# Kernel optimization log

Hardware: AMD Instinct MI355X
Metric: run time of the kernel (lower is better)

## Reference

```python
import jax, jax.numpy as jnp
import numpy as np

B, S, D, H = 8, 1024, 1024, 16
DK = D // H


def setup_inputs() -> dict:
    key = jax.random.key(0)
    ks = jax.random.split(key, 10)
    scale = 1.0 / np.sqrt(D)
    return {
        "x": jax.random.normal(ks[0], (B, S, D), dtype=jnp.float32),
        "prefix": jax.random.randint(ks[1], (B,), 0, S, dtype=jnp.int32),
        "Wq": jax.random.normal(ks[2], (D, D), dtype=jnp.float32) * scale,
        "bq": jnp.zeros((D,), dtype=jnp.float32),
        "Wk": jax.random.normal(ks[3], (D, D), dtype=jnp.float32) * scale,
        "bk": jnp.zeros((D,), dtype=jnp.float32),
        "Wv": jax.random.normal(ks[4], (D, D), dtype=jnp.float32) * scale,
        "bv": jnp.zeros((D,), dtype=jnp.float32),
        "Wo": jax.random.normal(ks[5], (D, D), dtype=jnp.float32) * scale,
        "bo": jnp.zeros((D,), dtype=jnp.float32),
    }


def reference(x, prefix, Wq, bq, Wk, bk, Wv, bv, Wo, bo):
    b, s, d = x.shape
    h, dk = H, DK
    # projections -> [b, h, s, dk]
    def split_heads(t):
        return t.reshape(b, s, h, dk).transpose(0, 2, 1, 3)
    q = split_heads(x @ Wq + bq)
    k = split_heads(x @ Wk + bk)
    v = split_heads(x @ Wv + bv)
    # raw scores (no 1/sqrt(dk) scaling in the original)
    scores = jnp.einsum('bhqd,bhkd->bhqk', q, k)
    # mask construction (faithful to original, incl. final permute/transpose):
    # allowed[b, q, k] = (q < prefix[b]) or (k >= q)
    q_idx = jnp.arange(s)[:, None]   # [s, 1]
    k_idx = jnp.arange(s)[None, :]   # [1, s]
    allowed = (q_idx[None, :, :] < prefix[:, None, None]) | (k_idx >= q_idx)  # [b, s, s]
    scores = jnp.where(allowed[:, None, :, :], scores, -jnp.inf)
    probs = jax.nn.softmax(scores, axis=-1)
    # einsum -> bqhd, then transpose(1,2) -> bhqd, then view(b, s, d) (faithful
    # to the original's head-interleaving reshape)
    out = jnp.einsum('bhql,bhld->bqhd', probs, v)
    out = out.transpose(0, 2, 1, 3).reshape(b, s, d)
    return out @ Wo + bo
```

## Files before the change

kernel.cpp:

```cpp
#include <hip/hip_runtime.h>
#include <stdint.h>

typedef __attribute__((ext_vector_type(8)))  short          short8;
typedef __attribute__((ext_vector_type(8)))  unsigned short u16x8;
typedef __attribute__((ext_vector_type(4)))  unsigned short u16x4;
typedef __attribute__((ext_vector_type(4)))  float          f32x4;
typedef __attribute__((ext_vector_type(16))) float          f32x16;

__device__ __forceinline__ unsigned short f2bf(float x) {
  unsigned int u = __float_as_uint(x);
  u += 0x7fffu + ((u >> 16) & 1u);
  return (unsigned short)(u >> 16);
}
__device__ __forceinline__ float bf2f(unsigned short b) {
  return __uint_as_float(((unsigned int)b) << 16);
}

__device__ __forceinline__ void mfma16(f32x4& c, short8 a, short8 b) {
  asm volatile("v_mfma_f32_16x16x32_bf16 %0, %1, %2, %0" : "+v"(c) : "v"(a), "v"(b));
}
__device__ __forceinline__ void mfma32(f32x16& c, short8 a, short8 b) {
  asm volatile("v_mfma_f32_32x32x16_bf16 %0, %1, %2, %0" : "+v"(c) : "v"(a), "v"(b));
}
__device__ __forceinline__ float hw_exp2(float x) {
  float r;
  asm("v_exp_f32 %0, %1" : "=v"(r) : "v"(x));
  return r;
}

#define GLDS(gsrc, ldst)                                                    \
  __builtin_amdgcn_global_load_lds(                                         \
      (const __attribute__((address_space(1))) void*)(gsrc),                \
      (__attribute__((address_space(3))) void*)(ldst), 16, 0, 0)

__global__ void split_x_kernel(const float4* __restrict__ x,
                               ushort4* __restrict__ xh, int n4) {
  int stride = gridDim.x * blockDim.x;
  for (int i = blockIdx.x * blockDim.x + threadIdx.x; i < n4; i += stride) {
    float4 v = x[i];
    ushort4 h;
    h.x = f2bf(v.x);
    h.y = f2bf(v.y);
    h.z = f2bf(v.z);
    h.w = f2bf(v.w);
    xh[i] = h;
  }
}

__global__ void wsplit_kernel(const float* __restrict__ Wq, const float* __restrict__ Wk,
                              const float* __restrict__ Wv, const float* __restrict__ Wo,
                              unsigned short* qk, unsigned short* vh, unsigned short* oh) {
  __shared__ float tile[32][33];
  int z = blockIdx.z;
  const float* W = (z == 0) ? Wq : (z == 1) ? Wk : (z == 2) ? Wv : Wo;
  unsigned short* Oh = (z == 0) ? qk : (z == 1) ? qk + (size_t)1024 * 1024
                      : (z == 2) ? vh : oh;
  int k0 = blockIdx.y * 32, n0 = blockIdx.x * 32;
  int tx = threadIdx.x & 31, ty = threadIdx.x >> 5;
#pragma unroll
  for (int j = 0; j < 4; ++j)
    tile[ty + 8 * j][tx] = W[(size_t)(k0 + ty + 8 * j) * 1024 + n0 + tx];
  __syncthreads();
#pragma unroll
  for (int j = 0; j < 4; ++j) {
    float v = tile[tx][ty + 8 * j];
    size_t idx = (size_t)(n0 + ty + 8 * j) * 1024 + k0 + tx;
    Oh[idx] = f2bf(v);
  }
}

template <int OUTMODE>
__global__ __launch_bounds__(256)
void gemm_kernel(const unsigned short* __restrict__ Ah,
                 const unsigned short* __restrict__ Bh,
                 const float* __restrict__ bias, const float* __restrict__ bias2,
                 unsigned short* __restrict__ Ch,
                 float* __restrict__ Cf, int M, int N, int K) {
  constexpr int SMEM = (OUTMODE == 3) ? (128 * 136) : (2 * 8192);
  __shared__ unsigned short smem[SMEM];
  unsigned short* sAh = smem;
  unsigned short* sBh = smem + 8192;

  int t = threadIdx.x;
  int wid = t >> 6, l = t & 63;
  int wm = wid >> 1, wn = wid & 1;
  int bm = blockIdx.y * 128, bn = blockIdx.x * 128;

  f32x4 acc[4][4] = {};

  for (int k0 = 0; k0 < K; k0 += 64) {
#pragma unroll
    for (int r = 0; r < 4; ++r) {
      int o = (r * 256 + t) << 4;
      int row = o >> 7;
      int gce = ((o & 127) ^ ((row & 7) << 4)) >> 1;
      int wb  = (o & ~1023) >> 1;
      size_t gA = (size_t)(bm + row) * K + k0 + gce;
      size_t gB = (size_t)(bn + row) * K + k0 + gce;
      GLDS(Ah + gA, sAh + wb);
      GLDS(Bh + gB, sBh + wb);
    }
    __syncthreads();
#pragma unroll
    for (int kh = 0; kh < 2; ++kh) {
      short8 afh[4], bfh[4];
#pragma unroll
      for (int m = 0; m < 4; ++m) {
        int row = wm * 64 + m * 16 + (l & 15);
        int cb = (((l >> 4) * 16 + kh * 64) ^ ((row & 7) << 4)) >> 1;
        afh[m] = *(const short8*)(sAh + row * 64 + cb);
      }
#pragma unroll
      for (int n = 0; n < 4; ++n) {
        int row = wn * 64 + n * 16 + (l & 15);
        int cb = (((l >> 4) * 16 + kh * 64) ^ ((row & 7) << 4)) >> 1;
        bfh[n] = *(const short8*)(sBh + row * 64 + cb);
      }
#pragma unroll
      for (int m = 0; m < 4; ++m)
#pragma unroll
        for (int n = 0; n < 4; ++n)
          mfma16(acc[m][n], afh[m], bfh[n]);
    }
    __syncthreads();
  }

  if (OUTMODE == 3) {
    unsigned short* sT = smem;
#pragma unroll
    for (int m = 0; m < 4; ++m) {
      int lrow0 = wm * 64 + m * 16 + (l >> 4) * 4;
#pragma unroll
      for (int n = 0; n < 4; ++n) {
        int lcol = wn * 64 + n * 16 + (l & 15);
        float bs = bias[bn + lcol];
        u16x4 w;
#pragma unroll
        for (int r = 0; r < 4; ++r) w[r] = f2bf(acc[m][n][r] + bs);
        *(u16x4*)&sT[lcol * 136 + lrow0] = w;
      }
    }
    __syncthreads();
#pragma unroll
    for (int j = 0; j < 8; ++j) {
      int c = (t >> 4) + 16 * j;
      int r = (t & 15) * 8;
      *(u16x8*)(Ch + (size_t)(bn + c) * M + bm + r) = *(const u16x8*)&sT[c * 136 + r];
    }
    return;
  }

#pragma unroll
  for (int m = 0; m < 4; ++m) {
    int grow0 = bm + wm * 64 + m * 16 + (l >> 4) * 4;
#pragma unroll
    for (int n = 0; n < 4; ++n) {
      int gcol = bn + wn * 64 + n * 16 + (l & 15);
      float bs = (bias2 && gcol >= 1024) ? bias2[gcol - 1024] : bias[gcol];
#pragma unroll
      for (int r = 0; r < 4; ++r) {
        float v = acc[m][n][r] + bs;
        size_t idx = (size_t)(grow0 + r) * N + gcol;
        if (OUTMODE == 2) Cf[idx] = v;
        else              Ch[idx] = f2bf(v);
      }
    }
  }
}

__global__ __launch_bounds__(128)
void attn_kernel(const unsigned short* __restrict__ QK,
                 const unsigned short* __restrict__ VT, const int* __restrict__ prefix,
                 unsigned short* __restrict__ AOh) {
  const float NEG = -3.0e38f;
  const float L2E = 1.4426950408889634f;
  const float MC  = 46.16624410f;
  __shared__ unsigned short sKh[2][32][66];
  __shared__ unsigned short sV [2][64][34];

  int bh = blockIdx.x;
  int b = bh >> 4, h = bh & 15;
  int t = threadIdx.x, wid = t >> 6, l = t & 63;
  int qb0 = blockIdx.y * 64;
  int qb = qb0 + wid * 32;
  int P = prefix[b];
  int lq = l & 31, g = l >> 5;
  int q = qb + lq;
  bool qfull = (q < P);
  bool allfull = (P >= qb + 32);

  short8 bqh[4];
  {
    size_t base = (size_t)(b * 1024 + q) * 2048 + h * 64 + g * 8;
#pragma unroll
    for (int c = 0; c < 4; ++c)
      bqh[c] = *(const short8*)(QK + base + c * 16);
  }

  const unsigned short* KhB = QK + (size_t)b * 1024 * 2048 + 1024 + h * 64;
  const unsigned short* VTB = VT + (size_t)(h * 64) * 8192 + b * 1024;

  int srow = t >> 3, scol = (t & 7) * 8;
  int vrow = t >> 2, vcol = (t & 3) * 8;

  int kt0 = (qb0 >= P) ? qb0 : 0;
  int ntiles = (1024 - kt0) >> 5;

  f32x16 o0 = {}, o1 = {};
  float lrun = 0.f;

  u16x8 rkh0, rkh1, rv0, rv1;
  rkh0 = *(const u16x8*)(KhB + (size_t)(kt0 + srow) * 2048 + scol);
  rkh1 = *(const u16x8*)(KhB + (size_t)(kt0 + srow + 16) * 2048 + scol);
  rv0  = *(const u16x8*)(VTB + (size_t)vrow * 8192 + kt0 + vcol);
  rv1  = *(const u16x8*)(VTB + (size_t)(vrow + 32) * 8192 + kt0 + vcol);
  *(u16x8*)&sKh[0][srow][scol]      = rkh0;
  *(u16x8*)&sKh[0][srow + 16][scol] = rkh1;
  *(u16x8*)&sV [0][vrow][vcol]      = rv0;
  *(u16x8*)&sV [0][vrow + 32][vcol] = rv1;
  __syncthreads();

  int cur = 0;
  for (int i = 0; i < ntiles; ++i) {
    int kt = kt0 + i * 32;
    bool more = (i + 1 < ntiles);
    if (more) {
      int ktn = kt + 32;
      rkh0 = *(const u16x8*)(KhB + (size_t)(ktn + srow) * 2048 + scol);
      rkh1 = *(const u16x8*)(KhB + (size_t)(ktn + srow + 16) * 2048 + scol);
      rv0  = *(const u16x8*)(VTB + (size_t)vrow * 8192 + ktn + vcol);
      rv1  = *(const u16x8*)(VTB + (size_t)(vrow + 32) * 8192 + ktn + vcol);
    }

    bool wave_dead = (qb >= P) && (kt + 31 < qb);
    if (!wave_dead) {
      f32x16 s = {};
      __builtin_amdgcn_s_setprio(1);
#pragma unroll
      for (int c = 0; c < 4; ++c) {
        short8 ah = *(const short8*)&sKh[cur][lq][g * 8 + c * 16];
        mfma32(s, ah, bqh[c]);
      }
      __builtin_amdgcn_s_setprio(0);

      float p[16];
      if (allfull || kt > qb) {
#pragma unroll
        for (int r = 0; r < 16; ++r)
          p[r] = hw_exp2(__builtin_fmaf(s[r], L2E, -MC));
      } else {
#pragma unroll
        for (int r = 0; r < 16; ++r) {
          int k = kt + (r & 3) + 8 * (r >> 2) + 4 * g;
          float sv = (qfull || k >= q) ? s[r] : NEG;
          p[r] = hw_exp2(__builtin_fmaf(sv, L2E, -MC));
        }
      }
      float s01 = p[0] + p[1],  s23 = p[2] + p[3],  s45 = p[4] + p[5],  s67 = p[6] + p[7];
      float s89 = p[8] + p[9],  sab = p[10] + p[11], scd = p[12] + p[13], sef = p[14] + p[15];
      lrun += ((s01 + s23) + (s45 + s67)) + ((s89 + sab) + (scd + sef));

      unsigned int w0, w1, w2, w3, w4, w5, w6, w7;
      asm("v_cvt_pk_bf16_f32 %0, %1, %2" : "=v"(w0) : "v"(p[0]),  "v"(p[1]));
      asm("v_cvt_pk_bf16_f32 %0, %1, %2" : "=v"(w1) : "v"(p[2]),  "v"(p[3]));
      asm("v_cvt_pk_bf16_f32 %0, %1, %2" : "=v"(w2) : "v"(p[4]),  "v"(p[5]));
      asm("v_cvt_pk_bf16_f32 %0, %1, %2" : "=v"(w3) : "v"(p[6]),  "v"(p[7]));
      asm("v_cvt_pk_bf16_f32 %0, %1, %2" : "=v"(w4) : "v"(p[8]),  "v"(p[9]));
      asm("v_cvt_pk_bf16_f32 %0, %1, %2" : "=v"(w5) : "v"(p[10]), "v"(p[11]));
      asm("v_cvt_pk_bf16_f32 %0, %1, %2" : "=v"(w6) : "v"(p[12]), "v"(p[13]));
      asm("v_cvt_pk_bf16_f32 %0, %1, %2" : "=v"(w7) : "v"(p[14]), "v"(p[15]));
      {
        unsigned int v0 = g ? w0 : w2, r0 = __shfl_xor(v0, 32);
        unsigned int v1 = g ? w1 : w3, r1 = __shfl_xor(v1, 32);
        unsigned int v4 = g ? w4 : w6, r4 = __shfl_xor(v4, 32);
        unsigned int v5 = g ? w5 : w7, r5 = __shfl_xor(v5, 32);
        unsigned int n0 = g ? r0 : w0, n2 = g ? w2 : r0;
        unsigned int n1 = g ? r1 : w1, n3 = g ? w3 : r1;
        unsigned int n4 = g ? r4 : w4, n6 = g ? w6 : r4;
        unsigned int n5 = g ? r5 : w5, n7 = g ? w7 : r5;
        w0 = n0; w1 = n1; w2 = n2; w3 = n3; w4 = n4; w5 = n5; w6 = n6; w7 = n7;
      }
      union { unsigned int u[4]; short8 v; } B0, B1;
      B0.u[0] = w0; B0.u[1] = w1; B0.u[2] = w2; B0.u[3] = w3;
      B1.u[0] = w4; B1.u[1] = w5; B1.u[2] = w6; B1.u[3] = w7;

      short8 va00 = *(const short8*)&sV[cur][lq][g * 8];
      short8 va01 = *(const short8*)&sV[cur][lq][16 + g * 8];
      short8 va10 = *(const short8*)&sV[cur][32 + lq][g * 8];
      short8 va11 = *(const short8*)&sV[cur][32 + lq][16 + g * 8];
      __builtin_amdgcn_s_setprio(1);
      mfma32(o0, va00, B0.v);
      mfma32(o0, va01, B1.v);
      mfma32(o1, va10, B0.v);
      mfma32(o1, va11, B1.v);
      __builtin_amdgcn_s_setprio(0);
    }

    if (more) {
      *(u16x8*)&sKh[cur ^ 1][srow][scol]      = rkh0;
      *(u16x8*)&sKh[cur ^ 1][srow + 16][scol] = rkh1;
      *(u16x8*)&sV [cur ^ 1][vrow][vcol]      = rv0;
      *(u16x8*)&sV [cur ^ 1][vrow + 32][vcol] = rv1;
    }
    __syncthreads();
    cur ^= 1;
  }

  lrun += __shfl_xor(lrun, 32);

  float inv = 1.0f / lrun;
  size_t obase = (size_t)(b * 1024 + h * 64 + (q >> 4)) * 1024 + (q & 15) * 64;
#pragma unroll
  for (int tt = 0; tt < 4; ++tt) {
    u16x4 w0, w1;
#pragma unroll
    for (int j = 0; j < 4; ++j) {
      w0[j] = f2bf(o0[4 * tt + j] * inv);
      w1[j] = f2bf(o1[4 * tt + j] * inv);
    }
    *(u16x4*)(AOh + obase + 8 * tt + 4 * g)      = w0;
    *(u16x4*)(AOh + obase + 32 + 8 * tt + 4 * g) = w1;
  }
}

extern "C" void kernel_launch(void* const* d_in, const int* in_sizes, int n_in,
                              void* d_out, int out_size, void* d_ws, size_t ws_size,
                              hipStream_t stream) {
  (void)in_sizes; (void)n_in; (void)out_size;
  const float* x      = (const float*)d_in[0];
  const int*   prefix = (const int*)d_in[1];
  const float* Wq = (const float*)d_in[2];
  const float* bq = (const float*)d_in[3];
  const float* Wk = (const float*)d_in[4];
  const float* bk = (const float*)d_in[5];
  const float* Wv = (const float*)d_in[6];
  const float* bv = (const float*)d_in[7];
  const float* Wo = (const float*)d_in[8];
  const float* bo = (const float*)d_in[9];
  float* out = (float*)d_out;

  const size_t MBY = 1ull << 20;
  if (ws_size < 144 * MBY) return;
  char* ws = (char*)d_ws;
  unsigned short* xh   = (unsigned short*)(ws + 0 * MBY);
  unsigned short* wqk  = (unsigned short*)(ws + 32 * MBY);
  unsigned short* wvh  = (unsigned short*)(ws + 40 * MBY);
  unsigned short* woh  = (unsigned short*)(ws + 44 * MBY);
  unsigned short* QK   = (unsigned short*)(ws + 48 * MBY);
  unsigned short* AOh  = (unsigned short*)(ws + 112 * MBY);
  unsigned short* VT   = (unsigned short*)(ws + 128 * MBY);

  split_x_kernel<<<1024, 256, 0, stream>>>((const float4*)x, (ushort4*)xh, 8192 * 1024 / 4);
  wsplit_kernel<<<dim3(32, 32, 4), 256, 0, stream>>>(Wq, Wk, Wv, Wo, wqk, wvh, woh);
  gemm_kernel<0><<<dim3(16, 64), 256, 0, stream>>>(xh, wqk, bq, bk, QK, nullptr,
                                                   8192, 2048, 1024);
  gemm_kernel<3><<<dim3(8, 64), 256, 0, stream>>>(xh, wvh, bv, nullptr, VT, nullptr,
                                                  8192, 1024, 1024);
  attn_kernel<<<dim3(128, 16), 128, 0, stream>>>(QK, VT, prefix, AOh);
  gemm_kernel<2><<<dim3(8, 64), 256, 0, stream>>>(AOh, woh, bo, nullptr, nullptr, out,
                                                  8192, 1024, 1024);
}
```

Measured before the change: 180.2 us.

## Fuse QKV projection GEMMs into one launch and deepen attention K/V prefetch

Combines the Q/K and V projection GEMMs into a single kernel over a concatenated weight buffer, branching on column block to write either the row-major QK output or the transposed V output. The attention loop now prefetches K/V tiles two iterations ahead using two alternating register sets, to hide global load latency further. This reduces launch count and tail imbalance, at the cost of more registers in attention and larger shared memory in the QK path.

```diff
diff --git a/kernel.cpp b/kernel.cpp
--- a/kernel.cpp
+++ b/kernel.cpp
@@ -49,12 +49,11 @@
 
 __global__ void wsplit_kernel(const float* __restrict__ Wq, const float* __restrict__ Wk,
                               const float* __restrict__ Wv, const float* __restrict__ Wo,
-                              unsigned short* qk, unsigned short* vh, unsigned short* oh) {
+                              unsigned short* qkv, unsigned short* oh) {
   __shared__ float tile[32][33];
   int z = blockIdx.z;
   const float* W = (z == 0) ? Wq : (z == 1) ? Wk : (z == 2) ? Wv : Wo;
-  unsigned short* Oh = (z == 0) ? qk : (z == 1) ? qk + (size_t)1024 * 1024
-                      : (z == 2) ? vh : oh;
+  unsigned short* Oh = (z < 3) ? qkv + (size_t)z * 1024 * 1024 : oh;
   int k0 = blockIdx.y * 32, n0 = blockIdx.x * 32;
   int tx = threadIdx.x & 31, ty = threadIdx.x >> 5;
 #pragma unroll
@@ -69,17 +68,16 @@
   }
 }
 
-template <int OUTMODE>
 __global__ __launch_bounds__(256)
-void gemm_kernel(const unsigned short* __restrict__ Ah,
-                 const unsigned short* __restrict__ Bh,
-                 const float* __restrict__ bias, const float* __restrict__ bias2,
-                 unsigned short* __restrict__ Ch,
-                 float* __restrict__ Cf, int M, int N, int K) {
-  constexpr int SMEM = (OUTMODE == 3) ? (128 * 136) : (2 * 8192);
-  __shared__ unsigned short smem[SMEM];
+void qkv_gemm_kernel(const unsigned short* __restrict__ Ah,
+                     const unsigned short* __restrict__ Bh,
+                     const float* __restrict__ bq, const float* __restrict__ bk,
+                     const float* __restrict__ bv,
+                     unsigned short* __restrict__ QK, unsigned short* __restrict__ VT) {
+  __shared__ unsigned short smem[128 * 136];
   unsigned short* sAh = smem;
   unsigned short* sBh = smem + 8192;
+  const int K = 1024, M = 8192;
 
   int t = threadIdx.x;
   int wid = t >> 6, l = t & 63;
@@ -125,7 +123,8 @@
     __syncthreads();
   }
 
-  if (OUTMODE == 3) {
+  if (bn >= 2048) {
+    int vb = bn - 2048;
     unsigned short* sT = smem;
 #pragma unroll
     for (int m = 0; m < 4; ++m) {
@@ -133,7 +132,7 @@
 #pragma unroll
       for (int n = 0; n < 4; ++n) {
         int lcol = wn * 64 + n * 16 + (l & 15);
-        float bs = bias[bn + lcol];
+        float bs = bv[vb + lcol];
         u16x4 w;
 #pragma unroll
         for (int r = 0; r < 4; ++r) w[r] = f2bf(acc[m][n][r] + bs);
@@ -145,7 +144,7 @@
     for (int j = 0; j < 8; ++j) {
       int c = (t >> 4) + 16 * j;
       int r = (t & 15) * 8;
-      *(u16x8*)(Ch + (size_t)(bn + c) * M + bm + r) = *(const u16x8*)&sT[c * 136 + r];
+      *(u16x8*)(VT + (size_t)(vb + c) * M + bm + r) = *(const u16x8*)&sT[c * 136 + r];
     }
     return;
   }
@@ -156,14 +155,76 @@
 #pragma unroll
     for (int n = 0; n < 4; ++n) {
       int gcol = bn + wn * 64 + n * 16 + (l & 15);
-      float bs = (bias2 && gcol >= 1024) ? bias2[gcol - 1024] : bias[gcol];
-#pragma unroll
-      for (int r = 0; r < 4; ++r) {
-        float v = acc[m][n][r] + bs;
-        size_t idx = (size_t)(grow0 + r) * N + gcol;
-        if (OUTMODE == 2) Cf[idx] = v;
-        else              Ch[idx] = f2bf(v);
-      }
+      float bs = (gcol < 1024) ? bq[gcol] : bk[gcol - 1024];
+#pragma unroll
+      for (int r = 0; r < 4; ++r)
+        QK[(size_t)(grow0 + r) * 2048 + gcol] = f2bf(acc[m][n][r] + bs);
+    }
+  }
+}
+
+__global__ __launch_bounds__(256)
+void gemm_out_kernel(const unsigned short* __restrict__ Ah,
+                     const unsigned short* __restrict__ Bh,
+                     const float* __restrict__ bias, float* __restrict__ Cf,
+                     int M, int N, int K) {
+  __shared__ unsigned short smem[2 * 8192];
+  unsigned short* sAh = smem;
+  unsigned short* sBh = smem + 8192;
+
+  int t = threadIdx.x;
+  int wid = t >> 6, l = t & 63;
+  int wm = wid >> 1, wn = wid & 1;
+  int bm = blockIdx.y * 128, bn = blockIdx.x * 128;
+
+  f32x4 acc[4][4] = {};
+
+  for (int k0 = 0; k0 < K; k0 += 64) {
+#pragma unroll
+    for (int r = 0; r < 4; ++r) {
+      int o = (r * 256 + t) << 4;
+      int row = o >> 7;
+      int gce = ((o & 127) ^ ((row & 7) << 4)) >> 1;
+      int wb  = (o & ~1023) >> 1;
+      size_t gA = (size_t)(bm + row) * K + k0 + gce;
+      size_t gB = (size_t)(bn + row) * K + k0 + gce;
+      GLDS(Ah + gA, sAh + wb);
+      GLDS(Bh + gB, sBh + wb);
+    }
+    __syncthreads();
+#pragma unroll
+    for (int kh = 0; kh < 2; ++kh) {
+      short8 afh[4], bfh[4];
+#pragma unroll
+      for (int m = 0; m < 4; ++m) {
+        int row = wm * 64 + m * 16 + (l & 15);
+        int cb = (((l >> 4) * 16 + kh * 64) ^ ((row & 7) << 4)) >> 1;
+        afh[m] = *(const short8*)(sAh + row * 64 + cb);
+      }
+#pragma unroll
+      for (int n = 0; n < 4; ++n) {
+        int row = wn * 64 + n * 16 + (l & 15);
+        int cb = (((l >> 4) * 16 + kh * 64) ^ ((row & 7) << 4)) >> 1;
+        bfh[n] = *(const short8*)(sBh + row * 64 + cb);
+      }
+#pragma unroll
+      for (int m = 0; m < 4; ++m)
+#pragma unroll
+        for (int n = 0; n < 4; ++n)
+          mfma16(acc[m][n], afh[m], bfh[n]);
+    }
+    __syncthreads();
+  }
+#pragma unroll
+  for (int m = 0; m < 4; ++m) {
+    int grow0 = bm + wm * 64 + m * 16 + (l >> 4) * 4;
+#pragma unroll
+    for (int n = 0; n < 4; ++n) {
+      int gcol = bn + wn * 64 + n * 16 + (l & 15);
+      float bs = bias[gcol];
+#pragma unroll
+      for (int r = 0; r < 4; ++r)
+        Cf[(size_t)(grow0 + r) * N + gcol] = acc[m][n][r] + bs;
     }
   }
 }
@@ -209,101 +270,129 @@
   f32x16 o0 = {}, o1 = {};
   float lrun = 0.f;
 
-  u16x8 rkh0, rkh1, rv0, rv1;
-  rkh0 = *(const u16x8*)(KhB + (size_t)(kt0 + srow) * 2048 + scol);
-  rkh1 = *(const u16x8*)(KhB + (size_t)(kt0 + srow + 16) * 2048 + scol);
-  rv0  = *(const u16x8*)(VTB + (size_t)vrow * 8192 + kt0 + vcol);
-  rv1  = *(const u16x8*)(VTB + (size_t)(vrow + 32) * 8192 + kt0 + vcol);
-  *(u16x8*)&sKh[0][srow][scol]      = rkh0;
-  *(u16x8*)&sKh[0][srow + 16][scol] = rkh1;
-  *(u16x8*)&sV [0][vrow][vcol]      = rv0;
-  *(u16x8*)&sV [0][vrow + 32][vcol] = rv1;
+  int cur = 0;
+  auto body = [&](int kt) {
+    bool wave_dead = (qb >= P) && (kt + 31 < qb);
+    if (wave_dead) return;
+    f32x16 s = {};
+    __builtin_amdgcn_s_setprio(1);
+#pragma unroll
+    for (int c = 0; c < 4; ++c) {
+      short8 ah = *(const short8*)&sKh[cur][lq][g * 8 + c * 16];
+      mfma32(s, ah, bqh[c]);
+    }
+    __builtin_amdgcn_s_setprio(0);
+
+    float p[16];
+    if (allfull || kt > qb) {
+#pragma unroll
+      for (int r = 0; r < 16; ++r)
+        p[r] = hw_exp2(__builtin_fmaf(s[r], L2E, -MC));
+    } else {
+#pragma unroll
+      for (int r = 0; r < 16; ++r) {
+        int k = kt + (r & 3) + 8 * (r >> 2) + 4 * g;
+        float sv = (qfull || k >= q) ? s[r] : NEG;
+        p[r] = hw_exp2(__builtin_fmaf(sv, L2E, -MC));
+      }
+    }
+    float s01 = p[0] + p[1],  s23 = p[2] + p[3],  s45 = p[4] + p[5],  s67 = p[6] + p[7];
+    float s89 = p[8] + p[9],  sab = p[10] + p[11], scd = p[12] + p[13], sef = p[14] + p[15];
+    lrun += ((s01 + s23) + (s45 + s67)) + ((s89 + sab) + (scd + sef));
+
+    unsigned int w0, w1, w2, w3, w4, w5, w6, w7;
+    asm("v_cvt_pk_bf16_f32 %0, %1, %2" : "=v"(w0) : "v"(p[0]),  "v"(p[1]));
+    asm("v_cvt_pk_bf16_f32 %0, %1, %2" : "=v"(w1) : "v"(p[2]),  "v"(p[3]));
+    asm("v_cvt_pk_bf16_f32 %0, %1, %2" : "=v"(w2) : "v"(p[4]),  "v"(p[5]));
+    asm("v_cvt_pk_bf16_f32 %0, %1, %2" : "=v"(w3) : "v"(p[6]),  "v"(p[7]));
+    asm("v_cvt_pk_bf16_f32 %0, %1, %2" : "=v"(w4) : "v"(p[8]),  "v"(p[9]));
+    asm("v_cvt_pk_bf16_f32 %0, %1, %2" : "=v"(w5) : "v"(p[10]), "v"(p[11]));
+    asm("v_cvt_pk_bf16_f32 %0, %1, %2" : "=v"(w6) : "v"(p[12]), "v"(p[13]));
+    asm("v_cvt_pk_bf16_f32 %0, %1, %2" : "=v"(w7) : "v"(p[14]), "v"(p[15]));
+    {
+      unsigned int v0 = g ? w0 : w2, r0 = __shfl_xor(v0, 32);
+      unsigned int v1 = g ? w1 : w3, r1 = __shfl_xor(v1, 32);
+      unsigned int v4 = g ? w4 : w6, r4 = __shfl_xor(v4, 32);
+      unsigned int v5 = g ? w5 : w7, r5 = __shfl_xor(v5, 32);
+      unsigned int n0 = g ? r0 : w0, n2 = g ? w2 : r0;
+      unsigned int n1 = g ? r1 : w1, n3 = g ? w3 : r1;
+      unsigned int n4 = g ? r4 : w4, n6 = g ? w6 : r4;
+      unsigned int n5 = g ? r5 : w5, n7 = g ? w7 : r5;
+      w0 = n0; w1 = n1; w2 = n2; w3 = n3; w4 = n4; w5 = n5; w6 = n6; w7 = n7;
+    }
+    union { unsigned int u[4]; short8 v; } B0, B1;
+    B0.u[0] = w0; B0.u[1] = w1; B0.u[2] = w2; B0.u[3] = w3;
+    B1.u[0] = w4; B1.u[1] = w5; B1.u[2] = w6; B1.u[3] = w7;
+
+    short8 va00 = *(const short8*)&sV[cur][lq][g * 8];
+    short8 va01 = *(const short8*)&sV[cur][lq][16 + g * 8];
+    short8 va10 = *(const short8*)&sV[cur][32 + lq][g * 8];
+    short8 va11 = *(const short8*)&sV[cur][32 + lq][16 + g * 8];
+    __builtin_amdgcn_s_setprio(1);
+    mfma32(o0, va00, B0.v);
+    mfma32(o0, va01, B1.v);
+    mfma32(o1, va10, B0.v);
+    mfma32(o1, va11, B1.v);
+    __builtin_amdgcn_s_setprio(0);
+  };
+
+  u16x8 akh0, akh1, av0, av1;
+  u16x8 bkh0, bkh1, bv0, bv1;
+  akh0 = *(const u16x8*)(KhB + (size_t)(kt0 + srow) * 2048 + scol);
+  akh1 = *(const u16x8*)(KhB + (size_t)(kt0 + srow + 16) * 2048 + scol);
+  av0  = *(const u16x8*)(VTB + (size_t)vrow * 8192 + kt0 + vcol);
+  av1  = *(const u16x8*)(VTB + (size_t)(vrow + 32) * 8192 + kt0 + vcol);
+  *(u16x8*)&sKh[0][srow][scol]      = akh0;
+  *(u16x8*)&sKh[0][srow + 16][scol] = akh1;
+  *(u16x8*)&sV [0][vrow][vcol]      = av0;
+  *(u16x8*)&sV [0][vrow + 32][vcol] = av1;
+  {
+    int kt1 = kt0 + ((1 < ntiles) ? 32 : 0);
+    akh0 = *(const u16x8*)(KhB + (size_t)(kt1 + srow) * 2048 + scol);
+    akh1 = *(const u16x8*)(KhB + (size_t)(kt1 + srow + 16) * 2048 + scol);
+    av0  = *(const u16x8*)(VTB + (size_t)vrow * 8192 + kt1 + vcol);
+    av1  = *(const u16x8*)(VTB + (size_t)(vrow + 32) * 8192 + kt1 + vcol);
+  }
   __syncthreads();
 
-  int cur = 0;
-  for (int i = 0; i < ntiles; ++i) {
-    int kt = kt0 + i * 32;
-    bool more = (i + 1 < ntiles);
-    if (more) {
-      int ktn = kt + 32;
-      rkh0 = *(const u16x8*)(KhB + (size_t)(ktn + srow) * 2048 + scol);
-      rkh1 = *(const u16x8*)(KhB + (size_t)(ktn + srow + 16) * 2048 + scol);
-      rv0  = *(const u16x8*)(VTB + (size_t)vrow * 8192 + ktn + vcol);
-      rv1  = *(const u16x8*)(VTB + (size_t)(vrow + 32) * 8192 + ktn + vcol);
-    }
-
-    bool wave_dead = (qb >= P) && (kt + 31 < qb);
-    if (!wave_dead) {
-      f32x16 s = {};
-      __builtin_amdgcn_s_setprio(1);
-#pragma unroll
-      for (int c = 0; c < 4; ++c) {
-        short8 ah = *(const short8*)&sKh[cur][lq][g * 8 + c * 16];
-        mfma32(s, ah, bqh[c]);
-      }
-      __builtin_amdgcn_s_setprio(0);
-
-      float p[16];
-      if (allfull || kt > qb) {
-#pragma unroll
-        for (int r = 0; r < 16; ++r)
-          p[r] = hw_exp2(__builtin_fmaf(s[r], L2E, -MC));
-      } else {
-#pragma unroll
-        for (int r = 0; r < 16; ++r) {
-          int k = kt + (r & 3) + 8 * (r >> 2) + 4 * g;
-          float sv = (qfull || k >= q) ? s[r] : NEG;
-          p[r] = hw_exp2(__builtin_fmaf(sv, L2E, -MC));
-        }
-      }
-      float s01 = p[0] + p[1],  s23 = p[2] + p[3],  s45 = p[4] + p[5],  s67 = p[6] + p[7];
-      float s89 = p[8] + p[9],  sab = p[10] + p[11], scd = p[12] + p[13], sef = p[14] + p[15];
-      lrun += ((s01 + s23) + (s45 + s67)) + ((s89 + sab) + (scd + sef));
-
-      unsigned int w0, w1, w2, w3, w4, w5, w6, w7;
-      asm("v_cvt_pk_bf16_f32 %0, %1, %2" : "=v"(w0) : "v"(p[0]),  "v"(p[1]));
-      asm("v_cvt_pk_bf16_f32 %0, %1, %2" : "=v"(w1) : "v"(p[2]),  "v"(p[3]));
-      asm("v_cvt_pk_bf16_f32 %0, %1, %2" : "=v"(w2) : "v"(p[4]),  "v"(p[5]));
-      asm("v_cvt_pk_bf16_f32 %0, %1, %2" : "=v"(w3) : "v"(p[6]),  "v"(p[7]));
-      asm("v_cvt_pk_bf16_f32 %0, %1, %2" : "=v"(w4) : "v"(p[8]),  "v"(p[9]));
-      asm("v_cvt_pk_bf16_f32 %0, %1, %2" : "=v"(w5) : "v"(p[10]), "v"(p[11]));
-      asm("v_cvt_pk_bf16_f32 %0, %1, %2" : "=v"(w6) : "v"(p[12]), "v"(p[13]));
-      asm("v_cvt_pk_bf16_f32 %0, %1, %2" : "=v"(w7) : "v"(p[14]), "v"(p[15]));
-      {
-        unsigned int v0 = g ? w0 : w2, r0 = __shfl_xor(v0, 32);
-        unsigned int v1 = g ? w1 : w3, r1 = __shfl_xor(v1, 32);
-        unsigned int v4 = g ? w4 : w6, r4 = __shfl_xor(v4, 32);
-        unsigned int v5 = g ? w5 : w7, r5 = __shfl_xor(v5, 32);
-        unsigned int n0 = g ? r0 : w0, n2 = g ? w2 : r0;
-        unsigned int n1 = g ? r1 : w1, n3 = g ? w3 : r1;
-        unsigned int n4 = g ? r4 : w4, n6 = g ? w6 : r4;
-        unsigned int n5 = g ? r5 : w5, n7 = g ? w7 : r5;
-        w0 = n0; w1 = n1; w2 = n2; w3 = n3; w4 = n4; w5 = n5; w6 = n6; w7 = n7;
-      }
-      union { unsigned int u[4]; short8 v; } B0, B1;
-      B0.u[0] = w0; B0.u[1] = w1; B0.u[2] = w2; B0.u[3] = w3;
-      B1.u[0] = w4; B1.u[1] = w5; B1.u[2] = w6; B1.u[3] = w7;
-
-      short8 va00 = *(const short8*)&sV[cur][lq][g * 8];
-      short8 va01 = *(const short8*)&sV[cur][lq][16 + g * 8];
-      short8 va10 = *(const short8*)&sV[cur][32 + lq][g * 8];
-      short8 va11 = *(const short8*)&sV[cur][32 + lq][16 + g * 8];
-      __builtin_amdgcn_s_setprio(1);
-      mfma32(o0, va00, B0.v);
-      mfma32(o0, va01, B1.v);
-      mfma32(o1, va10, B0.v);
-      mfma32(o1, va11, B1.v);
-      __builtin_amdgcn_s_setprio(0);
-    }
-
-    if (more) {
-      *(u16x8*)&sKh[cur ^ 1][srow][scol]      = rkh0;
-      *(u16x8*)&sKh[cur ^ 1][srow + 16][scol] = rkh1;
-      *(u16x8*)&sV [cur ^ 1][vrow][vcol]      = rv0;
-      *(u16x8*)&sV [cur ^ 1][vrow + 32][vcol] = rv1;
-    }
-    __syncthreads();
-    cur ^= 1;
+  int i = 0;
+  while (true) {
+    {
+      int i2 = (i + 2 < ntiles) ? (i + 2) : (ntiles - 1);
+      int kt2 = kt0 + i2 * 32;
+      bkh0 = *(const u16x8*)(KhB + (size_t)(kt2 + srow) * 2048 + scol);
+      bkh1 = *(const u16x8*)(KhB + (size_t)(kt2 + srow + 16) * 2048 + scol);
+      bv0  = *(const u16x8*)(VTB + (size_t)vrow * 8192 + kt2 + vcol);
+      bv1  = *(const u16x8*)(VTB + (size_t)(vrow + 32) * 8192 + kt2 + vcol);
+      body(kt0 + i * 32);
+      if (i + 1 < ntiles) {
+        *(u16x8*)&sKh[cur ^ 1][srow][scol]      = akh0;
+        *(u16x8*)&sKh[cur ^ 1][srow + 16][scol] = akh1;
+        *(u16x8*)&sV [cur ^ 1][vrow][vcol]      = av0;
+        *(u16x8*)&sV [cur ^ 1][vrow + 32][vcol] = av1;
+      }
+      __syncthreads();
+      cur ^= 1; ++i;
+      if (i >= ntiles) break;
+    }
+    {
+      int i2 = (i + 2 < ntiles) ? (i + 2) : (ntiles - 1);
+      int kt2 = kt0 + i2 * 32;
+      akh0 = *(const u16x8*)(KhB + (size_t)(kt2 + srow) * 2048 + scol);
+      akh1 = *(const u16x8*)(KhB + (size_t)(kt2 + srow + 16) * 2048 + scol);
+      av0  = *(const u16x8*)(VTB + (size_t)vrow * 8192 + kt2 + vcol);
+      av1  = *(const u16x8*)(VTB + (size_t)(vrow + 32) * 8192 + kt2 + vcol);
+      body(kt0 + i * 32);
+      if (i + 1 < ntiles) {
+        *(u16x8*)&sKh[cur ^ 1][srow][scol]      = bkh0;
+        *(u16x8*)&sKh[cur ^ 1][srow + 16][scol] = bkh1;
+        *(u16x8*)&sV [cur ^ 1][vrow][vcol]      = bv0;
+        *(u16x8*)&sV [cur ^ 1][vrow + 32][vcol] = bv1;
+      }
+      __syncthreads();
+      cur ^= 1; ++i;
+      if (i >= ntiles) break;
+    }
   }
 
   lrun += __shfl_xor(lrun, 32);
@@ -343,20 +432,15 @@
   if (ws_size < 144 * MBY) return;
   char* ws = (char*)d_ws;
   unsigned short* xh   = (unsigned short*)(ws + 0 * MBY);
-  unsigned short* wqk  = (unsigned short*)(ws + 32 * MBY);
-  unsigned short* wvh  = (unsigned short*)(ws + 40 * MBY);
+  unsigned short* wqkv = (unsigned short*)(ws + 32 * MBY);
   unsigned short* woh  = (unsigned short*)(ws + 44 * MBY);
   unsigned short* QK   = (unsigned short*)(ws + 48 * MBY);
   unsigned short* AOh  = (unsigned short*)(ws + 112 * MBY);
   unsigned short* VT   = (unsigned short*)(ws + 128 * MBY);
 
   split_x_kernel<<<1024, 256, 0, stream>>>((const float4*)x, (ushort4*)xh, 8192 * 1024 / 4);
-  wsplit_kernel<<<dim3(32, 32, 4), 256, 0, stream>>>(Wq, Wk, Wv, Wo, wqk, wvh, woh);
-  gemm_kernel<0><<<dim3(16, 64), 256, 0, stream>>>(xh, wqk, bq, bk, QK, nullptr,
-                                                   8192, 2048, 1024);
-  gemm_kernel<3><<<dim3(8, 64), 256, 0, stream>>>(xh, wvh, bv, nullptr, VT, nullptr,
-                                                  8192, 1024, 1024);
+  wsplit_kernel<<<dim3(32, 32, 4), 256, 0, stream>>>(Wq, Wk, Wv, Wo, wqkv, woh);
+  qkv_gemm_kernel<<<dim3(24, 64), 256, 0, stream>>>(xh, wqkv, bq, bk, bv, QK, VT);
   attn_kernel<<<dim3(128, 16), 128, 0, stream>>>(QK, VT, prefix, AOh);
-  gemm_kernel<2><<<dim3(8, 64), 256, 0, stream>>>(AOh, woh, bo, nullptr, nullptr, out,
-                                                  8192, 1024, 1024);
-}
+  gemm_out_kernel<<<dim3(8, 64), 256, 0, stream>>>(AOh, woh, bo, out, 8192, 1024, 1024);
+}
```

Measured after the change: 166.5 us (median of 2 runs). 1.08x faster.
